# Optimization experiments

Measured on AMD Instinct MI355X. Metric: run time of the kernel, lower is better.

Reference implementation:

```python
import jax, jax.numpy as jnp
import numpy as np

N_NODES = 100000
N_EDGES = 3200000


def setup_inputs() -> dict:
    key = jax.random.key(0)
    ks = jax.random.split(key, 8)
    x = jax.random.normal(ks[0], (N_NODES, 128), dtype=jnp.float32)
    edge_index = jax.random.randint(ks[1], (2, N_EDGES), 0, N_NODES, dtype=jnp.int64)
    edge_weight = jax.random.uniform(ks[2], (N_EDGES,), dtype=jnp.float32)
    W1 = jax.random.normal(ks[3], (128, 32), dtype=jnp.float32) * (1.0 / np.sqrt(128))
    b1 = jnp.zeros((32,), dtype=jnp.float32)
    W2 = jax.random.normal(ks[4], (32, 16), dtype=jnp.float32) * (1.0 / np.sqrt(32))
    b2 = jnp.zeros((16,), dtype=jnp.float32)
    Wfc = jax.random.normal(ks[5], (16, 1), dtype=jnp.float32) * (1.0 / np.sqrt(16))
    bfc = jnp.zeros((1,), dtype=jnp.float32)
    return {"x": x, "edge_index": edge_index, "edge_weight": edge_weight,
            "W1": W1, "b1": b1, "W2": W2, "b2": b2, "Wfc": Wfc, "bfc": bfc}


def _gcn_norm(edge_index, edge_weight, num_nodes):
    # PyG gcn_norm: add self-loops (weight 1), sym-normalize by in-degree of target (col)
    row, col = edge_index[0], edge_index[1]
    loop = jnp.arange(num_nodes, dtype=row.dtype)
    row_f = jnp.concatenate([row, loop])
    col_f = jnp.concatenate([col, loop])
    w_f = jnp.concatenate([edge_weight, jnp.ones((num_nodes,), edge_weight.dtype)])
    deg = jax.ops.segment_sum(w_f, col_f, num_segments=num_nodes)
    dinv = jnp.where(deg > 0, deg ** -0.5, 0.0)
    norm_w = dinv[row_f] * w_f * dinv[col_f]  # [E+N]
    return row_f, col_f, norm_w


def _gcn_conv(x, row_f, col_f, norm_w, W, b, num_nodes):
    h = x @ W                      # transform first (in->out dims)
    msg = h[row_f] * norm_w[:, None]  # gather source features, scale by edge norm
    out = jax.ops.segment_sum(msg, col_f, num_segments=num_nodes)  # scatter-add to targets
    return out + b


def reference(x, edge_index, edge_weight, W1, b1, W2, b2, Wfc, bfc):
    N = x.shape[0]
    row_f, col_f, norm_w = _gcn_norm(edge_index, edge_weight, N)
    h = jax.nn.leaky_relu(_gcn_conv(x, row_f, col_f, norm_w, W1, b1, N))
    # dropout is identity in eval mode; norm=False skips GraphNorm
    h = jax.nn.leaky_relu(_gcn_conv(h, row_f, col_f, norm_w, W2, b2, N))
    return h @ Wfc + bfc  # [N, 1]
```

## Files before the change

### kernel.cpp

```cpp
#include <hip/hip_runtime.h>
#include <hip/hip_fp16.h>

#define N_NODES 100000
#define N_EDGES 3200000
#define BSHIFT 7
#define BSIZE 128
#define NB ((N_NODES + BSIZE - 1) / BSIZE)
#define CAP 4736
#define ROWBITS 17
#define ROWMASK ((1 << ROWBITS) - 1)
#define EPB 8192
#define NBLOCKS ((N_EDGES + EPB - 1) / EPB)


__global__ void k_detect(const unsigned* __restrict__ w, int* __restrict__ flag) {
    __shared__ unsigned s[256];
    unsigned v = 0;
    for (int t = threadIdx.x; t < 4096; t += 256) v |= w[2 * t + 1];
    s[threadIdx.x] = v;
    __syncthreads();
    for (int off = 128; off > 0; off >>= 1) {
        if (threadIdx.x < (unsigned)off) s[threadIdx.x] |= s[threadIdx.x + off];
        __syncthreads();
    }
    if (threadIdx.x == 0) flag[0] = (s[0] == 0) ? 1 : 0;
}

__device__ __forceinline__ void load_edge(const unsigned* __restrict__ e, int f, int E,
                                          int i, int& r, int& c) {
    if (f) { r = (int)e[2 * i]; c = (int)e[2 * E + 2 * i]; }
    else   { r = (int)e[i];     c = (int)e[E + i]; }
}


__global__ __launch_bounds__(512) void k_scatter(const unsigned* __restrict__ eidx,
                                                 const int* __restrict__ flag,
                                                 const float* __restrict__ ew,
                                                 int2* __restrict__ staged,
                                                 int* __restrict__ cntT,
                                                 int* __restrict__ offT, int E, int n) {
    __shared__ int2 se[EPB];
    __shared__ int  hist[NB];
    __shared__ int  bpos[NB];
    __shared__ int  s2[512];
    int tid = threadIdx.x;
    int blk = blockIdx.x;
    for (int i = tid; i < NB; i += 512) hist[i] = 0;
    __syncthreads();
    int f = flag[0];
    int base = blk * EPB;
    int lim = min(EPB, E - base);
    int rr[16], cc[16];
    float wv[16];
#pragma unroll
    for (int k = 0; k < 16; ++k) {
        int i = k * 512 + tid;
        rr[k] = -1; cc[k] = 0; wv[k] = 0.f;
        if (i < lim) {
            int r, c;
            load_edge(eidx, f, E, base + i, r, c);
            if ((unsigned)r < (unsigned)n && (unsigned)c < (unsigned)n) {
                rr[k] = r; cc[k] = c; wv[k] = ew[base + i];
            }
        }
    }
#pragma unroll
    for (int k = 0; k < 16; ++k)
        if (rr[k] >= 0) atomicAdd(&hist[cc[k] >> BSHIFT], 1);
    __syncthreads();
    int c0 = (2 * tid < NB) ? hist[2 * tid] : 0;
    int c1 = (2 * tid + 1 < NB) ? hist[2 * tid + 1] : 0;
    s2[tid] = c0 + c1;
    __syncthreads();
    for (int o = 1; o < 512; o <<= 1) {
        int t = (tid >= o) ? s2[tid - o] : 0;
        __syncthreads();
        s2[tid] += t;
        __syncthreads();
    }
    int cbase = s2[tid] - (c0 + c1);
    if (2 * tid < NB) bpos[2 * tid] = cbase;
    if (2 * tid + 1 < NB) bpos[2 * tid + 1] = cbase + c0;
    __syncthreads();
    for (int b = tid; b < NB; b += 512) {
        cntT[(size_t)blk * NB + b] = hist[b];
        offT[(size_t)blk * NB + b] = bpos[b];
    }
    __syncthreads();
#pragma unroll
    for (int k = 0; k < 16; ++k) {
        if (rr[k] >= 0) {
            int b = cc[k] >> BSHIFT, off = cc[k] & (BSIZE - 1);
            int pos = atomicAdd(&bpos[b], 1);
            se[pos] = make_int2((off << ROWBITS) | rr[k], __float_as_int(wv[k]));
        }
    }
    __syncthreads();
    for (int i = tid; i < lim; i += 512)
        staged[(size_t)blk * EPB + i] = se[i];
}


__global__ __launch_bounds__(256) void k_passb(const int2* __restrict__ staged,
                                               const int* __restrict__ cntT,
                                               const int* __restrict__ offT,
                                               int2* __restrict__ erw,
                                               int* __restrict__ start,
                                               int* __restrict__ end,
                                               float* __restrict__ dinv, int n) {
    __shared__ int   rdst[NBLOCKS + 1];
    __shared__ int   rsrc[NBLOCKS];
    __shared__ int   s2[256];
    __shared__ int   cnt[256];
    __shared__ float wsm[BSIZE];
    __shared__ int   cur[BSIZE];
    int tid = threadIdx.x;
    int b = blockIdx.x;
    int n0 = b << BSHIFT;
    int nn = min(BSIZE, n - n0);
    size_t bb = (size_t)b * CAP;
    int c0 = 0, c1 = 0;
    {
        int j0 = 2 * tid, j1 = 2 * tid + 1;
        if (j0 < NBLOCKS) {
            c0 = cntT[(size_t)j0 * NB + b];
            rsrc[j0] = j0 * EPB + offT[(size_t)j0 * NB + b];
        }
        if (j1 < NBLOCKS) {
            c1 = cntT[(size_t)j1 * NB + b];
            rsrc[j1] = j1 * EPB + offT[(size_t)j1 * NB + b];
        }
    }
    s2[tid] = c0 + c1;
    cnt[tid] = 0;
    if (tid < BSIZE) wsm[tid] = 0.f;
    __syncthreads();
    for (int o = 1; o < 256; o <<= 1) {
        int t = (tid >= o) ? s2[tid - o] : 0;
        __syncthreads();
        s2[tid] += t;
        __syncthreads();
    }
    int cbase = s2[tid] - (c0 + c1);
    if (2 * tid < NBLOCKS) rdst[2 * tid] = cbase;
    if (2 * tid + 1 < NBLOCKS) rdst[2 * tid + 1] = cbase + c0;
    if (tid == 255) rdst[NBLOCKS] = s2[255];
    __syncthreads();
    int cntE = min(rdst[NBLOCKS], CAP);
    for (int d = tid; d < cntE; d += 256) {
        int lo = 0, hi = NBLOCKS;
        while (hi - lo > 1) {
            int mid = (lo + hi) >> 1;
            if (rdst[mid] <= d) lo = mid; else hi = mid;
        }
        int2 kv = staged[(size_t)rsrc[lo] + (d - rdst[lo])];
        int off = kv.x >> ROWBITS;
        atomicAdd(&cnt[off], 1);
        atomicAdd(&wsm[off], __int_as_float(kv.y));
    }
    __syncthreads();
    int v = cnt[tid];
    for (int o = 1; o < 256; o <<= 1) {
        int t = (tid >= o) ? cnt[tid - o] : 0;
        __syncthreads();
        cnt[tid] += t;
        __syncthreads();
    }
    int excl = cnt[tid] - v;
    if (tid < nn) {
        start[n0 + tid] = (int)bb + excl;
        end[n0 + tid]   = (int)bb + excl + v;
        dinv[n0 + tid]  = 1.0f / sqrtf(1.0f + wsm[tid]);
    }
    if (tid < BSIZE) cur[tid] = excl;
    __syncthreads();
    for (int d = tid; d < cntE; d += 256) {
        int lo = 0, hi = NBLOCKS;
        while (hi - lo > 1) {
            int mid = (lo + hi) >> 1;
            if (rdst[mid] <= d) lo = mid; else hi = mid;
        }
        int2 kv = staged[(size_t)rsrc[lo] + (d - rdst[lo])];
        int off = kv.x >> ROWBITS;
        int p = atomicAdd(&cur[off], 1);
        erw[bb + p] = make_int2(kv.x & ROWMASK, kv.y);
    }
}


__global__ __launch_bounds__(256) void k_gemm1(const float* __restrict__ x,
                                               const float* __restrict__ W1,
                                               const float* __restrict__ dinv,
                                               __half* __restrict__ g1, int n) {
    __shared__ float W1s[128 * 32];
    __shared__ float xs[8][128];
    int tid = threadIdx.x;
    for (int i = tid; i < 1024; i += 256)
        *reinterpret_cast<float4*>(W1s + 4 * i) = reinterpret_cast<const float4*>(W1)[i];
    int node0 = blockIdx.x * 8;
    {
        int ln = tid >> 5, ii = tid & 31;
        int node = node0 + ln;
        float4 vv = make_float4(0.f, 0.f, 0.f, 0.f);
        if (node < n) vv = reinterpret_cast<const float4*>(x)[node * 32 + ii];
        *reinterpret_cast<float4*>(&xs[ln][4 * ii]) = vv;
    }
    __syncthreads();
    int ln = tid >> 5;
    int kk = tid & 31;
    int node = node0 + ln;
    if (node < n) {
        float acc = 0.f;
#pragma unroll
        for (int i = 0; i < 128; ++i) acc += xs[ln][i] * W1s[i * 32 + kk];
        g1[node * 32 + kk] = __float2half(dinv[node] * acc);
    }
}


__global__ __launch_bounds__(256) void k_agg1(const __half* __restrict__ g,
                                              const int* __restrict__ start,
                                              const int* __restrict__ end,
                                              const int2* __restrict__ erw,
                                              const float* __restrict__ dinv,
                                              const float* __restrict__ b1,
                                              float* __restrict__ h, int n) {
    int wid = (blockIdx.x * 256 + threadIdx.x) >> 6;
    int l = threadIdx.x & 63;
    if (wid >= n) return;
    int slot = l >> 3;
    int cg   = l & 7;
    int s = start[wid], en = end[wid];
    float4 acc = make_float4(0.f, 0.f, 0.f, 0.f);
    for (int e0 = s; e0 < en; e0 += 8) {
        int e = e0 + slot;
        bool ok = e < en;
        int2 rw = erw[ok ? e : s];
        float w = ok ? __int_as_float(rw.y) : 0.f;
        float2 raw = *reinterpret_cast<const float2*>(g + ((size_t)rw.x << 5) + (cg << 2));
        __half2 h01 = *reinterpret_cast<const __half2*>(&raw.x);
        __half2 h23 = *reinterpret_cast<const __half2*>(&raw.y);
        float2 f01 = __half22float2(h01), f23 = __half22float2(h23);
        acc.x += w * f01.x; acc.y += w * f01.y;
        acc.z += w * f23.x; acc.w += w * f23.y;
    }
#pragma unroll
    for (int m = 8; m <= 32; m <<= 1) {
        acc.x += __shfl_xor(acc.x, m);
        acc.y += __shfl_xor(acc.y, m);
        acc.z += __shfl_xor(acc.z, m);
        acc.w += __shfl_xor(acc.w, m);
    }
    if (slot == 0) {
        float2 raw = *reinterpret_cast<const float2*>(g + ((size_t)wid << 5) + (cg << 2));
        __half2 h01 = *reinterpret_cast<const __half2*>(&raw.x);
        __half2 h23 = *reinterpret_cast<const __half2*>(&raw.y);
        float2 f01 = __half22float2(h01), f23 = __half22float2(h23);
        float di = dinv[wid];
        float4 b = *reinterpret_cast<const float4*>(b1 + (cg << 2));
        float4 v;
        v.x = di * (acc.x + f01.x) + b.x;
        v.y = di * (acc.y + f01.y) + b.y;
        v.z = di * (acc.z + f23.x) + b.z;
        v.w = di * (acc.w + f23.y) + b.w;
        v.x = v.x > 0.f ? v.x : 0.01f * v.x;
        v.y = v.y > 0.f ? v.y : 0.01f * v.y;
        v.z = v.z > 0.f ? v.z : 0.01f * v.z;
        v.w = v.w > 0.f ? v.w : 0.01f * v.w;
        *reinterpret_cast<float4*>(h + ((size_t)wid << 5) + (cg << 2)) = v;
    }
}


__global__ __launch_bounds__(256) void k_gemm2(const float* __restrict__ h1,
                                               const float* __restrict__ W2,
                                               const float* __restrict__ dinv,
                                               __half* __restrict__ g2, int n) {
    __shared__ float W2s[32 * 16];
    int tid = threadIdx.x;
    for (int i = tid; i < 32 * 16; i += 256) W2s[i] = W2[i];
    __syncthreads();
    int t = blockIdx.x * 256 + tid;
    if (t < n * 16) {
        int node = t >> 4, j = t & 15;
        float acc = 0.f;
#pragma unroll
        for (int k = 0; k < 32; ++k) acc += h1[node * 32 + k] * W2s[k * 16 + j];
        g2[t] = __float2half(dinv[node] * acc);
    }
}


__global__ __launch_bounds__(256) void k_agg2(const __half* __restrict__ g2,
                                              const int* __restrict__ start,
                                              const int* __restrict__ end,
                                              const int2* __restrict__ erw,
                                              const float* __restrict__ dinv,
                                              const float* __restrict__ b2,
                                              const float* __restrict__ Wfc,
                                              const float* __restrict__ bfc,
                                              float* __restrict__ out, int n) {
    int wid = (blockIdx.x * 256 + threadIdx.x) >> 6;
    int l = threadIdx.x & 63;
    if (wid >= n) return;
    int slot = l >> 2;
    int cg   = l & 3;
    int s = start[wid], en = end[wid];
    float4 acc = make_float4(0.f, 0.f, 0.f, 0.f);
    for (int e0 = s; e0 < en; e0 += 16) {
        int e = e0 + slot;
        bool ok = e < en;
        int2 rw = erw[ok ? e : s];
        float w = ok ? __int_as_float(rw.y) : 0.f;
        float2 raw = *reinterpret_cast<const float2*>(g2 + ((size_t)rw.x << 4) + (cg << 2));
        __half2 h01 = *reinterpret_cast<const __half2*>(&raw.x);
        __half2 h23 = *reinterpret_cast<const __half2*>(&raw.y);
        float2 f01 = __half22float2(h01), f23 = __half22float2(h23);
        acc.x += w * f01.x; acc.y += w * f01.y;
        acc.z += w * f23.x; acc.w += w * f23.y;
    }
#pragma unroll
    for (int m = 4; m <= 32; m <<= 1) {
        acc.x += __shfl_xor(acc.x, m);
        acc.y += __shfl_xor(acc.y, m);
        acc.z += __shfl_xor(acc.z, m);
        acc.w += __shfl_xor(acc.w, m);
    }
    float2 raw = *reinterpret_cast<const float2*>(g2 + ((size_t)wid << 4) + (cg << 2));
    __half2 h01 = *reinterpret_cast<const __half2*>(&raw.x);
    __half2 h23 = *reinterpret_cast<const __half2*>(&raw.y);
    float2 f01 = __half22float2(h01), f23 = __half22float2(h23);
    float di = dinv[wid];
    float4 b = *reinterpret_cast<const float4*>(b2 + (cg << 2));
    float4 wf = *reinterpret_cast<const float4*>(Wfc + (cg << 2));
    float4 v;
    v.x = di * (acc.x + f01.x) + b.x;
    v.y = di * (acc.y + f01.y) + b.y;
    v.z = di * (acc.z + f23.x) + b.z;
    v.w = di * (acc.w + f23.y) + b.w;
    v.x = v.x > 0.f ? v.x : 0.01f * v.x;
    v.y = v.y > 0.f ? v.y : 0.01f * v.y;
    v.z = v.z > 0.f ? v.z : 0.01f * v.z;
    v.w = v.w > 0.f ? v.w : 0.01f * v.w;
    float p = v.x * wf.x + v.y * wf.y + v.z * wf.z + v.w * wf.w;
    p += __shfl_xor(p, 1);
    p += __shfl_xor(p, 2);
    if (l == 0) out[wid] = p + bfc[0];
}

extern "C" void kernel_launch(void* const* d_in, const int* in_sizes, int n_in,
                              void* d_out, int out_size, void* d_ws, size_t ws_size,
                              hipStream_t stream) {
    const float*    x    = (const float*)d_in[0];
    const unsigned* eidx = (const unsigned*)d_in[1];
    const float*    ew   = (const float*)d_in[2];
    const float*    W1   = (const float*)d_in[3];
    const float*    b1   = (const float*)d_in[4];
    const float*    W2   = (const float*)d_in[5];
    const float*    b2   = (const float*)d_in[6];
    const float*    Wfc  = (const float*)d_in[7];
    const float*    bfc  = (const float*)d_in[8];
    float* out = (float*)d_out;

    const int N = N_NODES;
    const int E = N_EDGES;

    char* ws = (char*)d_ws;
    int*    flag   = (int*)ws;
    int*    start  = (int*)(ws + 64u * 1024);
    int*    end    = (int*)(ws + 512u * 1024);
    float*  dinv   = (float*)(ws + 1024u * 1024);
    int*    cntT   = (int*)(ws + 1536u * 1024);
    int*    offT   = (int*)(ws + 2816u * 1024);
    int2*   staged = (int2*)(ws + 4u * 1024 * 1024);
    int2*   erw    = (int2*)(ws + 30u * 1024 * 1024);
    __half* g1h    = (__half*)(ws + 4u * 1024 * 1024);
    float*  h1     = (float*)(ws + 11u * 1024 * 1024);
    __half* g2h    = (__half*)(ws + 24u * 1024 * 1024);

    k_detect<<<1, 256, 0, stream>>>(eidx, flag);

    k_scatter<<<NBLOCKS, 512, 0, stream>>>(eidx, flag, ew, staged, cntT, offT, E, N);
    k_passb<<<NB, 256, 0, stream>>>(staged, cntT, offT, erw, start, end, dinv, N);

    k_gemm1<<<(N + 7) / 8, 256, 0, stream>>>(x, W1, dinv, g1h, N);
    {
        int blocks = (int)(((long long)N * 64 + 255) / 256);
        k_agg1<<<blocks, 256, 0, stream>>>(g1h, start, end, erw, dinv, b1, h1, N);
    }

    k_gemm2<<<(N * 16 + 255) / 256, 256, 0, stream>>>(h1, W2, dinv, g2h, N);
    {
        int blocks = (int)(((long long)N * 64 + 255) / 256);
        k_agg2<<<blocks, 256, 0, stream>>>(g2h, start, end, erw, dinv, b2, Wfc, bfc, out, N);
    }
}
```

Baseline: 370.3 us.

## Aggregate directly from bucket-staged edges with LDS atomics, dropping CSR build

Removes the second pass of k_passb that built a per-node CSR (start/end/erw). Both aggregation kernels now process one 128-node bucket per block, reading the staged edges straight from the scatter output and accumulating messages into shared-memory tiles with atomic adds before the epilogue. This saves one full rewrite of the edge list and the per-node prefix scans. In exchange it adds a binary search per edge in every aggregation pass and heavy LDS float atomic contention. Parallelism also drops to about 782 blocks, and summation order becomes nondeterministic.

```diff
diff --git a/kernel.cpp b/kernel.cpp
--- a/kernel.cpp
+++ b/kernel.cpp
@@ -6,7 +6,6 @@
 #define BSHIFT 7
 #define BSIZE 128
 #define NB ((N_NODES + BSIZE - 1) / BSIZE)
-#define CAP 4736
 #define ROWBITS 17
 #define ROWMASK ((1 << ROWBITS) - 1)
 #define EPB 8192
@@ -101,90 +100,61 @@
 }
 
 
-__global__ __launch_bounds__(256) void k_passb(const int2* __restrict__ staged,
-                                               const int* __restrict__ cntT,
-                                               const int* __restrict__ offT,
-                                               int2* __restrict__ erw,
-                                               int* __restrict__ start,
-                                               int* __restrict__ end,
-                                               float* __restrict__ dinv, int n) {
+__device__ __forceinline__ int bucket_tables(const int* __restrict__ cntT,
+                                             const int* __restrict__ offT,
+                                             int b, int* rdst, int* rsrc, int* s2) {
+    int tid = threadIdx.x;
+    int c0 = 0, c1 = 0;
+    int j0 = 2 * tid, j1 = 2 * tid + 1;
+    if (j0 < NBLOCKS) { c0 = cntT[(size_t)j0 * NB + b]; rsrc[j0] = j0 * EPB + offT[(size_t)j0 * NB + b]; }
+    if (j1 < NBLOCKS) { c1 = cntT[(size_t)j1 * NB + b]; rsrc[j1] = j1 * EPB + offT[(size_t)j1 * NB + b]; }
+    s2[tid] = c0 + c1;
+    __syncthreads();
+    for (int o = 1; o < 256; o <<= 1) {
+        int t = (tid >= o) ? s2[tid - o] : 0;
+        __syncthreads();
+        s2[tid] += t;
+        __syncthreads();
+    }
+    int cbase = s2[tid] - (c0 + c1);
+    if (j0 < NBLOCKS) rdst[j0] = cbase;
+    if (j1 < NBLOCKS) rdst[j1] = cbase + c0;
+    if (tid == 255) rdst[NBLOCKS] = s2[255];
+    __syncthreads();
+    return rdst[NBLOCKS];
+}
+
+__device__ __forceinline__ int run_search(const int* __restrict__ rdst, int d) {
+    int lo = 0, hi = NBLOCKS;
+    while (hi - lo > 1) {
+        int mid = (lo + hi) >> 1;
+        if (rdst[mid] <= d) lo = mid; else hi = mid;
+    }
+    return lo;
+}
+
+
+__global__ __launch_bounds__(256) void k_dinv(const int2* __restrict__ staged,
+                                              const int* __restrict__ cntT,
+                                              const int* __restrict__ offT,
+                                              float* __restrict__ dinv, int n) {
     __shared__ int   rdst[NBLOCKS + 1];
     __shared__ int   rsrc[NBLOCKS];
     __shared__ int   s2[256];
-    __shared__ int   cnt[256];
     __shared__ float wsm[BSIZE];
-    __shared__ int   cur[BSIZE];
     int tid = threadIdx.x;
     int b = blockIdx.x;
     int n0 = b << BSHIFT;
     int nn = min(BSIZE, n - n0);
-    size_t bb = (size_t)b * CAP;
-    int c0 = 0, c1 = 0;
-    {
-        int j0 = 2 * tid, j1 = 2 * tid + 1;
-        if (j0 < NBLOCKS) {
-            c0 = cntT[(size_t)j0 * NB + b];
-            rsrc[j0] = j0 * EPB + offT[(size_t)j0 * NB + b];
-        }
-        if (j1 < NBLOCKS) {
-            c1 = cntT[(size_t)j1 * NB + b];
-            rsrc[j1] = j1 * EPB + offT[(size_t)j1 * NB + b];
-        }
-    }
-    s2[tid] = c0 + c1;
-    cnt[tid] = 0;
     if (tid < BSIZE) wsm[tid] = 0.f;
-    __syncthreads();
-    for (int o = 1; o < 256; o <<= 1) {
-        int t = (tid >= o) ? s2[tid - o] : 0;
-        __syncthreads();
-        s2[tid] += t;
-        __syncthreads();
-    }
-    int cbase = s2[tid] - (c0 + c1);
-    if (2 * tid < NBLOCKS) rdst[2 * tid] = cbase;
-    if (2 * tid + 1 < NBLOCKS) rdst[2 * tid + 1] = cbase + c0;
-    if (tid == 255) rdst[NBLOCKS] = s2[255];
-    __syncthreads();
-    int cntE = min(rdst[NBLOCKS], CAP);
+    int cntE = bucket_tables(cntT, offT, b, rdst, rsrc, s2);
     for (int d = tid; d < cntE; d += 256) {
-        int lo = 0, hi = NBLOCKS;
-        while (hi - lo > 1) {
-            int mid = (lo + hi) >> 1;
-            if (rdst[mid] <= d) lo = mid; else hi = mid;
-        }
+        int lo = run_search(rdst, d);
         int2 kv = staged[(size_t)rsrc[lo] + (d - rdst[lo])];
-        int off = kv.x >> ROWBITS;
-        atomicAdd(&cnt[off], 1);
-        atomicAdd(&wsm[off], __int_as_float(kv.y));
-    }
-    __syncthreads();
-    int v = cnt[tid];
-    for (int o = 1; o < 256; o <<= 1) {
-        int t = (tid >= o) ? cnt[tid - o] : 0;
-        __syncthreads();
-        cnt[tid] += t;
-        __syncthreads();
-    }
-    int excl = cnt[tid] - v;
-    if (tid < nn) {
-        start[n0 + tid] = (int)bb + excl;
-        end[n0 + tid]   = (int)bb + excl + v;
-        dinv[n0 + tid]  = 1.0f / sqrtf(1.0f + wsm[tid]);
-    }
-    if (tid < BSIZE) cur[tid] = excl;
-    __syncthreads();
-    for (int d = tid; d < cntE; d += 256) {
-        int lo = 0, hi = NBLOCKS;
-        while (hi - lo > 1) {
-            int mid = (lo + hi) >> 1;
-            if (rdst[mid] <= d) lo = mid; else hi = mid;
-        }
-        int2 kv = staged[(size_t)rsrc[lo] + (d - rdst[lo])];
-        int off = kv.x >> ROWBITS;
-        int p = atomicAdd(&cur[off], 1);
-        erw[bb + p] = make_int2(kv.x & ROWMASK, kv.y);
-    }
+        atomicAdd(&wsm[kv.x >> ROWBITS], __int_as_float(kv.y));
+    }
+    __syncthreads();
+    if (tid < nn) dinv[n0 + tid] = 1.0f / sqrtf(1.0f + wsm[tid]);
 }
 
 
@@ -218,56 +188,48 @@
 }
 
 
-__global__ __launch_bounds__(256) void k_agg1(const __half* __restrict__ g,
-                                              const int* __restrict__ start,
-                                              const int* __restrict__ end,
-                                              const int2* __restrict__ erw,
+__global__ __launch_bounds__(256) void k_agg1(const int2* __restrict__ staged,
+                                              const int* __restrict__ cntT,
+                                              const int* __restrict__ offT,
+                                              const __half* __restrict__ g,
                                               const float* __restrict__ dinv,
                                               const float* __restrict__ b1,
                                               float* __restrict__ h, int n) {
-    int wid = (blockIdx.x * 256 + threadIdx.x) >> 6;
-    int l = threadIdx.x & 63;
-    if (wid >= n) return;
-    int slot = l >> 3;
-    int cg   = l & 7;
-    int s = start[wid], en = end[wid];
-    float4 acc = make_float4(0.f, 0.f, 0.f, 0.f);
-    for (int e0 = s; e0 < en; e0 += 8) {
-        int e = e0 + slot;
-        bool ok = e < en;
-        int2 rw = erw[ok ? e : s];
-        float w = ok ? __int_as_float(rw.y) : 0.f;
-        float2 raw = *reinterpret_cast<const float2*>(g + ((size_t)rw.x << 5) + (cg << 2));
+    __shared__ int   rdst[NBLOCKS + 1];
+    __shared__ int   rsrc[NBLOCKS];
+    __shared__ int   s2[256];
+    __shared__ float acc[BSIZE][33];
+    int tid = threadIdx.x;
+    int b = blockIdx.x;
+    int n0 = b << BSHIFT;
+    int nn = min(BSIZE, n - n0);
+    for (int i = tid; i < BSIZE * 33; i += 256) (&acc[0][0])[i] = 0.f;
+    int cntE = bucket_tables(cntT, offT, b, rdst, rsrc, s2);
+    int grp = tid >> 3;
+    int cg  = tid & 7;
+    for (int d = grp; d < cntE; d += 32) {
+        int lo = run_search(rdst, d);
+        int2 kv = staged[(size_t)rsrc[lo] + (d - rdst[lo])];
+        int off = kv.x >> ROWBITS;
+        int row = kv.x & ROWMASK;
+        float w = __int_as_float(kv.y);
+        float2 raw = *reinterpret_cast<const float2*>(g + ((size_t)row << 5) + (cg << 2));
         __half2 h01 = *reinterpret_cast<const __half2*>(&raw.x);
         __half2 h23 = *reinterpret_cast<const __half2*>(&raw.y);
         float2 f01 = __half22float2(h01), f23 = __half22float2(h23);
-        acc.x += w * f01.x; acc.y += w * f01.y;
-        acc.z += w * f23.x; acc.w += w * f23.y;
-    }
-#pragma unroll
-    for (int m = 8; m <= 32; m <<= 1) {
-        acc.x += __shfl_xor(acc.x, m);
-        acc.y += __shfl_xor(acc.y, m);
-        acc.z += __shfl_xor(acc.z, m);
-        acc.w += __shfl_xor(acc.w, m);
-    }
-    if (slot == 0) {
-        float2 raw = *reinterpret_cast<const float2*>(g + ((size_t)wid << 5) + (cg << 2));
-        __half2 h01 = *reinterpret_cast<const __half2*>(&raw.x);
-        __half2 h23 = *reinterpret_cast<const __half2*>(&raw.y);
-        float2 f01 = __half22float2(h01), f23 = __half22float2(h23);
-        float di = dinv[wid];
-        float4 b = *reinterpret_cast<const float4*>(b1 + (cg << 2));
-        float4 v;
-        v.x = di * (acc.x + f01.x) + b.x;
-        v.y = di * (acc.y + f01.y) + b.y;
-        v.z = di * (acc.z + f23.x) + b.z;
-        v.w = di * (acc.w + f23.y) + b.w;
-        v.x = v.x > 0.f ? v.x : 0.01f * v.x;
-        v.y = v.y > 0.f ? v.y : 0.01f * v.y;
-        v.z = v.z > 0.f ? v.z : 0.01f * v.z;
-        v.w = v.w > 0.f ? v.w : 0.01f * v.w;
-        *reinterpret_cast<float4*>(h + ((size_t)wid << 5) + (cg << 2)) = v;
+        atomicAdd(&acc[off][(cg << 2) + 0], w * f01.x);
+        atomicAdd(&acc[off][(cg << 2) + 1], w * f01.y);
+        atomicAdd(&acc[off][(cg << 2) + 2], w * f23.x);
+        atomicAdd(&acc[off][(cg << 2) + 3], w * f23.y);
+    }
+    __syncthreads();
+    for (int idx = tid; idx < nn * 32; idx += 256) {
+        int node = idx >> 5, k = idx & 31;
+        float self = __half2float(g[((size_t)(n0 + node) << 5) + k]);
+        float di = dinv[n0 + node];
+        float v = di * (acc[node][k] + self) + b1[k];
+        v = v > 0.f ? v : 0.01f * v;
+        h[((size_t)(n0 + node) << 5) + k] = v;
     }
 }
 
@@ -291,61 +253,56 @@
 }
 
 
-__global__ __launch_bounds__(256) void k_agg2(const __half* __restrict__ g2,
-                                              const int* __restrict__ start,
-                                              const int* __restrict__ end,
-                                              const int2* __restrict__ erw,
+__global__ __launch_bounds__(256) void k_agg2(const int2* __restrict__ staged,
+                                              const int* __restrict__ cntT,
+                                              const int* __restrict__ offT,
+                                              const __half* __restrict__ g2,
                                               const float* __restrict__ dinv,
                                               const float* __restrict__ b2,
                                               const float* __restrict__ Wfc,
                                               const float* __restrict__ bfc,
                                               float* __restrict__ out, int n) {
-    int wid = (blockIdx.x * 256 + threadIdx.x) >> 6;
-    int l = threadIdx.x & 63;
-    if (wid >= n) return;
-    int slot = l >> 2;
-    int cg   = l & 3;
-    int s = start[wid], en = end[wid];
-    float4 acc = make_float4(0.f, 0.f, 0.f, 0.f);
-    for (int e0 = s; e0 < en; e0 += 16) {
-        int e = e0 + slot;
-        bool ok = e < en;
-        int2 rw = erw[ok ? e : s];
-        float w = ok ? __int_as_float(rw.y) : 0.f;
-        float2 raw = *reinterpret_cast<const float2*>(g2 + ((size_t)rw.x << 4) + (cg << 2));
+    __shared__ int   rdst[NBLOCKS + 1];
+    __shared__ int   rsrc[NBLOCKS];
+    __shared__ int   s2[256];
+    __shared__ float acc[BSIZE][17];
+    int tid = threadIdx.x;
+    int b = blockIdx.x;
+    int n0 = b << BSHIFT;
+    int nn = min(BSIZE, n - n0);
+    for (int i = tid; i < BSIZE * 17; i += 256) (&acc[0][0])[i] = 0.f;
+    int cntE = bucket_tables(cntT, offT, b, rdst, rsrc, s2);
+    int grp = tid >> 2;
+    int cg  = tid & 3;
+    for (int d = grp; d < cntE; d += 64) {
+        int lo = run_search(rdst, d);
+        int2 kv = staged[(size_t)rsrc[lo] + (d - rdst[lo])];
+        int off = kv.x >> ROWBITS;
+        int row = kv.x & ROWMASK;
+        float w = __int_as_float(kv.y);
+        float2 raw = *reinterpret_cast<const float2*>(g2 + ((size_t)row << 4) + (cg << 2));
         __half2 h01 = *reinterpret_cast<const __half2*>(&raw.x);
         __half2 h23 = *reinterpret_cast<const __half2*>(&raw.y);
         float2 f01 = __half22float2(h01), f23 = __half22float2(h23);
-        acc.x += w * f01.x; acc.y += w * f01.y;
-        acc.z += w * f23.x; acc.w += w * f23.y;
-    }
-#pragma unroll
-    for (int m = 4; m <= 32; m <<= 1) {
-        acc.x += __shfl_xor(acc.x, m);
-        acc.y += __shfl_xor(acc.y, m);
-        acc.z += __shfl_xor(acc.z, m);
-        acc.w += __shfl_xor(acc.w, m);
-    }
-    float2 raw = *reinterpret_cast<const float2*>(g2 + ((size_t)wid << 4) + (cg << 2));
-    __half2 h01 = *reinterpret_cast<const __half2*>(&raw.x);
-    __half2 h23 = *reinterpret_cast<const __half2*>(&raw.y);
-    float2 f01 = __half22float2(h01), f23 = __half22float2(h23);
-    float di = dinv[wid];
-    float4 b = *reinterpret_cast<const float4*>(b2 + (cg << 2));
-    float4 wf = *reinterpret_cast<const float4*>(Wfc + (cg << 2));
-    float4 v;
-    v.x = di * (acc.x + f01.x) + b.x;
-    v.y = di * (acc.y + f01.y) + b.y;
-    v.z = di * (acc.z + f23.x) + b.z;
-    v.w = di * (acc.w + f23.y) + b.w;
-    v.x = v.x > 0.f ? v.x : 0.01f * v.x;
-    v.y = v.y > 0.f ? v.y : 0.01f * v.y;
-    v.z = v.z > 0.f ? v.z : 0.01f * v.z;
-    v.w = v.w > 0.f ? v.w : 0.01f * v.w;
-    float p = v.x * wf.x + v.y * wf.y + v.z * wf.z + v.w * wf.w;
-    p += __shfl_xor(p, 1);
-    p += __shfl_xor(p, 2);
-    if (l == 0) out[wid] = p + bfc[0];
+        atomicAdd(&acc[off][(cg << 2) + 0], w * f01.x);
+        atomicAdd(&acc[off][(cg << 2) + 1], w * f01.y);
+        atomicAdd(&acc[off][(cg << 2) + 2], w * f23.x);
+        atomicAdd(&acc[off][(cg << 2) + 3], w * f23.y);
+    }
+    __syncthreads();
+    if (tid < nn) {
+        int node = tid;
+        float di = dinv[n0 + node];
+        float p = 0.f;
+#pragma unroll
+        for (int j = 0; j < 16; ++j) {
+            float self = __half2float(g2[((size_t)(n0 + node) << 4) + j]);
+            float v = di * (acc[node][j] + self) + b2[j];
+            v = v > 0.f ? v : 0.01f * v;
+            p += v * Wfc[j];
+        }
+        out[n0 + node] = p + bfc[0];
+    }
 }
 
 extern "C" void kernel_launch(void* const* d_in, const int* in_sizes, int n_in,
@@ -367,31 +324,22 @@
 
     char* ws = (char*)d_ws;
     int*    flag   = (int*)ws;
-    int*    start  = (int*)(ws + 64u * 1024);
-    int*    end    = (int*)(ws + 512u * 1024);
     float*  dinv   = (float*)(ws + 1024u * 1024);
     int*    cntT   = (int*)(ws + 1536u * 1024);
     int*    offT   = (int*)(ws + 2816u * 1024);
     int2*   staged = (int2*)(ws + 4u * 1024 * 1024);
-    int2*   erw    = (int2*)(ws + 30u * 1024 * 1024);
-    __half* g1h    = (__half*)(ws + 4u * 1024 * 1024);
-    float*  h1     = (float*)(ws + 11u * 1024 * 1024);
-    __half* g2h    = (__half*)(ws + 24u * 1024 * 1024);
+    __half* g1h    = (__half*)(ws + 30u * 1024 * 1024);
+    float*  h1     = (float*)(ws + 37u * 1024 * 1024);
+    __half* g2h    = (__half*)(ws + 50u * 1024 * 1024);
 
     k_detect<<<1, 256, 0, stream>>>(eidx, flag);
 
     k_scatter<<<NBLOCKS, 512, 0, stream>>>(eidx, flag, ew, staged, cntT, offT, E, N);
-    k_passb<<<NB, 256, 0, stream>>>(staged, cntT, offT, erw, start, end, dinv, N);
+    k_dinv<<<NB, 256, 0, stream>>>(staged, cntT, offT, dinv, N);
 
     k_gemm1<<<(N + 7) / 8, 256, 0, stream>>>(x, W1, dinv, g1h, N);
-    {
-        int blocks = (int)(((long long)N * 64 + 255) / 256);
-        k_agg1<<<blocks, 256, 0, stream>>>(g1h, start, end, erw, dinv, b1, h1, N);
-    }
+    k_agg1<<<NB, 256, 0, stream>>>(staged, cntT, offT, g1h, dinv, b1, h1, N);
 
     k_gemm2<<<(N * 16 + 255) / 256, 256, 0, stream>>>(h1, W2, dinv, g2h, N);
-    {
-        int blocks = (int)(((long long)N * 64 + 255) / 256);
-        k_agg2<<<blocks, 256, 0, stream>>>(g2h, start, end, erw, dinv, b2, Wfc, bfc, out, N);
-    }
-}
+    k_agg2<<<NB, 256, 0, stream>>>(staged, cntT, offT, g2h, dinv, b2, Wfc, bfc, out, N);
+}
```

Result: slower. 1.404 ms (+279.1%).
